# Performance work log

Measured on AMD Instinct MI355X. Metric: run time of the kernel, lower is better.

## Reference

```python
import jax, jax.numpy as jnp
import numpy as np

WS = 32      # window_size
P = 4        # patch size inside window
HEADS = 8
DIM_HEAD = 64
INNER = HEADS * DIM_HEAD  # 512
SCALE = DIM_HEAD ** -0.5


def setup_inputs() -> dict:
    key = jax.random.key(0)
    k1, k2, k3 = jax.random.split(key, 3)
    B, C, S = 8, 64, 256
    token_dim = P * P * C  # 1024
    x = jax.random.normal(k1, (B, C, S, S), dtype=jnp.float32)
    w_qkv = jax.random.normal(k2, (token_dim, 3 * INNER), dtype=jnp.float32) * (token_dim ** -0.5)
    w_out = jax.random.normal(k3, (INNER, token_dim), dtype=jnp.float32) * (INNER ** -0.5)
    b_out = jnp.zeros((token_dim,), dtype=jnp.float32)
    return {"x": x, "w_qkv": w_qkv, "w_out": w_out, "b_out": b_out}


def reference(x, w_qkv, w_out, b_out):
    B, C, H, W = x.shape
    H1, W1 = H // WS, W // WS
    # --- divide_regions: b c (h1 h) (w1 w) -> (b h1 w1) c h w ---
    xw = x.reshape(B, C, H1, WS, W1, WS).transpose(0, 2, 4, 1, 3, 5)
    xw = xw.reshape(B * H1 * W1, C, WS, WS)          # [n, C, ws, ws]
    n = xw.shape[0]
    nh = WS // P                                      # patches per side
    # patchify window: n c (nh p1) (nw p2) -> n (nh nw) (p1 p2 c)
    t = xw.reshape(n, C, nh, P, nh, P).transpose(0, 2, 4, 3, 5, 1)
    tokens = t.reshape(n, nh * nh, P * P * C)         # [n, T, D]
    # --- attention ---
    qkv = jnp.einsum('ntd,de->nte', tokens, w_qkv)    # [n, T, 3*inner]
    q, k, v = jnp.split(qkv, 3, axis=-1)
    def heads(a):
        return a.reshape(n, -1, HEADS, DIM_HEAD).transpose(0, 2, 1, 3)  # [n,h,T,dh]
    q, k, v = heads(q), heads(k), heads(v)
    attn = jax.nn.softmax(jnp.einsum('nhqd,nhkd->nhqk', q, k) * SCALE, axis=-1)
    o = jnp.einsum('nhqk,nhkd->nhqd', attn, v)        # [n,h,T,dh]
    o = o.transpose(0, 2, 1, 3).reshape(n, nh * nh, INNER)
    o = jnp.einsum('nte,ed->ntd', o, w_out) + b_out   # [n, T, D]
    # un-patchify: n (nh nw) (p1 p2 c) -> n c (nh p1) (nw p2)
    o = o.reshape(n, nh, nh, P, P, C).transpose(0, 5, 1, 3, 2, 4)
    o = o.reshape(n, C, WS, WS)
    # --- combine_regions: (b h1 w1) c h w -> b c (h1 h) (w1 w) ---
    o = o.reshape(B, H1, W1, C, WS, WS).transpose(0, 3, 1, 4, 2, 5)
    return o.reshape(B, C, H, W)
```

## Files before the change

### kernel.cpp

```cpp
#include <hip/hip_runtime.h>
#include <hip/hip_bf16.h>
#include <stdint.h>

typedef __attribute__((ext_vector_type(8))) short short8;
typedef __attribute__((ext_vector_type(4))) float floatx4;

constexpr int TD    = 1024;
constexpr int E3    = 1536;
constexpr int INNER = 512;
constexpr int NW    = 512;
constexpr int M_    = NW * 64;


constexpr size_t OFF_TOKA = 0;
constexpr size_t OFF_QKV  = (size_t)M_ * TD * 2;
constexpr size_t OFF_WQT  = OFF_QKV + (size_t)M_ * E3 * 2;
constexpr size_t OFF_WOT  = OFF_WQT + (size_t)E3 * TD * 2;
constexpr size_t OFF_BO   = OFF_WOT + (size_t)TD * INNER * 2;
constexpr size_t WS_NEED  = OFF_BO + TD * 4;

__device__ __forceinline__ void gl_lds16(const void* g, void* l) {
  __builtin_amdgcn_global_load_lds(
      (const __attribute__((address_space(1))) void*)g,
      (__attribute__((address_space(3))) void*)l, 16, 0, 0);
}

__global__ __launch_bounds__(256) void k_patchify(const float* __restrict__ x,
                                                  __hip_bfloat16* __restrict__ tokA) {
  __shared__ __hip_bfloat16 tok[8][1032];
  const int bid = blockIdx.x;
  const int n = bid >> 3, i = bid & 7;
  const int b = n >> 6, h1 = (n >> 3) & 7, w1 = n & 7;
  const int tid = threadIdx.x;
  for (int it = 0; it < 8; ++it) {
    int idx = it * 256 + tid;
    int w4 = idx & 7, p1 = (idx >> 3) & 3, c = idx >> 5;
    int h = h1 * 32 + i * 4 + p1;
    const float4 v = *(const float4*)&x[(((b * 64 + c) * 256 + h) * 256 + w1 * 32 + w4 * 4)];
    __hip_bfloat16* dst = &tok[w4][c * 16 + p1 * 4];
    dst[0] = __float2bfloat16(v.x);
    dst[1] = __float2bfloat16(v.y);
    dst[2] = __float2bfloat16(v.z);
    dst[3] = __float2bfloat16(v.w);
  }
  __syncthreads();
  for (int it = 0; it < 4; ++it) {
    int idx = it * 256 + tid;
    int ch = idx & 127, j = idx >> 7;
    uint4 v = *(const uint4*)&tok[j][ch * 8];
    *(uint4*)&tokA[(size_t)(n * 64 + i * 8 + j) * 1024 + ch * 8] = v;
  }
}

__global__ __launch_bounds__(256) void k_perm_wqkv(const float* __restrict__ wqkv,
                                                   __hip_bfloat16* __restrict__ wqT) {
  __shared__ __hip_bfloat16 wt[16][520];
  const int e0 = blockIdx.x * 16, by = blockIdx.y, tid = threadIdx.x;
  for (int it = 0; it < 32; ++it) {
    int idx = it * 256 + tid;
    int e = idx & 15, dl = idx >> 4;
    int d = by * 512 + dl;
    float v = wqkv[d * 1536 + e0 + e];
    int c = d & 63, off = (d >> 6) & 7;
    wt[e][c * 8 + off] = __float2bfloat16(v);
  }
  __syncthreads();
  for (int it = 0; it < 4; ++it) {
    int idx = it * 256 + tid;
    int ch = idx & 63, e = idx >> 6;
    uint4 v = *(const uint4*)&wt[e][ch * 8];
    *(uint4*)&wqT[(size_t)(e0 + e) * 1024 + ch * 16 + by * 8] = v;
  }
}

__global__ __launch_bounds__(256) void k_perm_wout(const float* __restrict__ wout,
                                                   __hip_bfloat16* __restrict__ woT) {
  __shared__ __hip_bfloat16 wt[4][520];
  const int e0 = blockIdx.x * 4, by = blockIdx.y, tid = threadIdx.x;
  for (int it = 0; it < 8; ++it) {
    int idx = it * 256 + tid;
    int dl = idx & 511, e = idx >> 9;
    int d = by * 512 + dl;
    float v = wout[(e0 + e) * 1024 + d];
    int c = d & 63, off = (d >> 6) & 7;
    wt[e][c * 8 + off] = __float2bfloat16(v);
  }
  __syncthreads();
  for (int it = 0; it < 8; ++it) {
    int idx = it * 256 + tid;
    int e = idx & 3, sl = idx >> 2;
    int c = sl >> 3, off = sl & 7;
    int dp = c * 16 + by * 8 + off;
    woT[(size_t)dp * 512 + e0 + e] = wt[e][sl];
  }
}

__global__ __launch_bounds__(256) void k_perm_bias(const float* __restrict__ bout,
                                                   float* __restrict__ boP) {
  int dp = blockIdx.x * 256 + threadIdx.x;
  int c = dp >> 4, p1 = (dp >> 2) & 3, p2 = dp & 3;
  boP[dp] = bout[p1 * 256 + p2 * 64 + c];
}

template<int K>
__device__ __forceinline__ void gemm256_acc(
    const __hip_bfloat16* __restrict__ A,
    const __hip_bfloat16* __restrict__ Bt,
    int m0, int n0, int tid,
    __hip_bfloat16 (*As)[256][64], __hip_bfloat16 (*Bs)[256][64],
    floatx4 (&acc)[8][4])
{
  const int lane = tid & 63, wid = tid >> 6;
  const int wm = wid >> 2, wn = wid & 3;
  const int l15 = lane & 15, quad = lane >> 4;

  const int rl8 = tid >> 3;
  const int ch0 = (tid & 7) ^ (rl8 & 7);
  const __hip_bfloat16* Abase = A  + (size_t)(m0 + rl8) * K + ch0 * 8;
  const __hip_bfloat16* Bbase = Bt + (size_t)(n0 + rl8) * K + ch0 * 8;

  auto stageB = [&](int tile, int half, int buf) {
#pragma unroll
    for (int j = 0; j < 2; ++j)
      gl_lds16(Bbase + (size_t)(half * 128 + j * 64) * K + tile * 64,
               (char*)&Bs[buf][0][0] + half * 16384 + (j * 512 + tid) * 16);
  };
  auto stageA = [&](int tile, int chunk, int buf) {
#pragma unroll
    for (int j = 0; j < 2; ++j)
      gl_lds16(Abase + (size_t)(j * 128 + chunk * 64) * K + tile * 64,
               (char*)&As[buf][0][0] + j * 16384 + chunk * 8192 + tid * 16);
  };

  short8 af[2][2][2];
  short8 bf[4][2];

#define VM6 asm volatile("s_waitcnt vmcnt(6)" ::: "memory")
#define VM0 asm volatile("s_waitcnt vmcnt(0)" ::: "memory")
#define LGKM4 do { asm volatile("s_waitcnt lgkmcnt(4)" ::: "memory"); \
                   __builtin_amdgcn_sched_barrier(0); } while (0)
#define LGKM0 do { asm volatile("s_waitcnt lgkmcnt(0)" ::: "memory"); \
                   __builtin_amdgcn_sched_barrier(0); } while (0)

#define PH(CS, QC, BUFC, LDB, QN, BUFN, PF, STAGE, VMW, LG)                       \
  do {                                                                            \
    if (LDB) {                              \
      _Pragma("unroll") for (int n = 0; n < 4; ++n) {                             \
        const int rb = wn * 64 + n * 16 + l15;                                    \
        _Pragma("unroll") for (int kh = 0; kh < 2; ++kh)                          \
          bf[n][kh] = *(const short8*)&Bs[BUFC][rb][((kh * 4 + quad) ^ (rb & 7)) * 8]; \
      }                                                                           \
    }                                                                             \
    if (PF) {                                                                     \
      _Pragma("unroll") for (int m2 = 0; m2 < 2; ++m2) {                          \
        const int r = wm * 128 + (2 * (QN) + m2) * 16 + l15;                      \
        _Pragma("unroll") for (int kh = 0; kh < 2; ++kh)                          \
          af[(CS) ^ 1][m2][kh] = *(const short8*)&As[BUFN][r][((kh * 4 + quad) ^ (r & 7)) * 8]; \
      }                                                                           \
    }                                                                             \
    STAGE;                                                                        \
    __builtin_amdgcn_sched_barrier(0);                                            \
    __builtin_amdgcn_s_barrier();                                                 \
    LG;                                                                           \
    __builtin_amdgcn_s_setprio(1);                                                \
    _Pragma("unroll") for (int kh = 0; kh < 2; ++kh)                              \
      _Pragma("unroll") for (int m2 = 0; m2 < 2; ++m2)                            \
        _Pragma("unroll") for (int n = 0; n < 4; ++n)                             \
          acc[2 * (QC) + m2][n] = __builtin_amdgcn_mfma_f32_16x16x32_bf16(        \
              af[CS][m2][kh], bf[n][kh], acc[2 * (QC) + m2][n], 0, 0, 0);         \
    __builtin_amdgcn_s_setprio(0);                                                \
    __builtin_amdgcn_sched_barrier(0);                                            \
    VMW;                                                                          \
    __builtin_amdgcn_s_barrier();                                                 \
    __builtin_amdgcn_sched_barrier(0);                                            \
  } while (0)

  stageB(0, 0, 0); stageB(0, 1, 0); stageA(0, 0, 0); stageA(0, 1, 0);
  stageB(1, 0, 1); stageB(1, 1, 1); stageA(1, 0, 1);
  VM6;
  __builtin_amdgcn_s_barrier();
  __builtin_amdgcn_sched_barrier(0);
#pragma unroll
  for (int m2 = 0; m2 < 2; ++m2) {
    const int r = wm * 128 + m2 * 16 + l15;
#pragma unroll
    for (int kh = 0; kh < 2; ++kh)
      af[0][m2][kh] = *(const short8*)&As[0][r][((kh * 4 + quad) ^ (r & 7)) * 8];
  }

  constexpr int NIT = K / 128;
#pragma unroll 1
  for (int i = 0; i < NIT - 1; ++i) {
    const int t1 = 2 * i + 1, t2 = 2 * i + 2, t3 = 2 * i + 3;
    PH(0, 0, 0, 1, 1, 0, 1, stageA(t1, 1, 1), VM6, LGKM4);
    PH(1, 1, 0, 0, 2, 0, 1, stageB(t2, 0, 0),    , LGKM4);
    PH(0, 2, 0, 0, 3, 0, 1, stageB(t2, 1, 0), VM6, LGKM4);
    PH(1, 3, 0, 0, 0, 1, 1, stageA(t2, 0, 0),    , LGKM4);
    PH(0, 0, 1, 1, 1, 1, 1, stageA(t2, 1, 0), VM6, LGKM4);
    PH(1, 1, 1, 0, 2, 1, 1, stageB(t3, 0, 1),    , LGKM4);
    PH(0, 2, 1, 0, 3, 1, 1, stageB(t3, 1, 1), VM6, LGKM4);
    PH(1, 3, 1, 0, 0, 0, 1, stageA(t3, 0, 1),    , LGKM4);
  }
  {
    const int tE = 2 * NIT - 1;
    PH(0, 0, 0, 1, 1, 0, 1, stageA(tE, 1, 1), VM6, LGKM4);
    PH(1, 1, 0, 0, 2, 0, 1, ,    , LGKM4);
    PH(0, 2, 0, 0, 3, 0, 1, , VM0, LGKM4);
    PH(1, 3, 0, 0, 0, 1, 1, ,    , LGKM4);
    PH(0, 0, 1, 1, 1, 1, 1, ,    , LGKM4);
    PH(1, 1, 1, 0, 2, 1, 1, ,    , LGKM4);
    PH(0, 2, 1, 0, 3, 1, 1, ,    , LGKM4);
    PH(1, 3, 1, 0, 0, 0, 0, ,    , LGKM0);
  }
#undef PH
#undef VM6
#undef VM0
#undef LGKM4
#undef LGKM0
}

__global__ __launch_bounds__(512, 2) void k_gemm_qkv(const __hip_bfloat16* __restrict__ A,
                                                     const __hip_bfloat16* __restrict__ Bt,
                                                     __hip_bfloat16* __restrict__ Cmat,
                                                     int lognb, int nbase) {
  __shared__ __hip_bfloat16 As[2][256][64];
  __shared__ __hip_bfloat16 Bs[2][256][64];
  const int tid = threadIdx.x;
  const int bid = blockIdx.x;
  const int cpx = gridDim.x >> 3;
  const int swz = (bid & 7) * cpx + (bid >> 3);
  const int nb1 = (1 << lognb) - 1;
  const int n0 = nbase + (swz & nb1) * 256, m0 = (swz >> lognb) * 256;
  floatx4 acc[8][4] = {};
  gemm256_acc<1024>(A, Bt, m0, n0, tid, As, Bs, acc);
  const int lane = tid & 63, wid = tid >> 6;
  const int wm = wid >> 2, wn = wid & 3;
  const int l15 = lane & 15, quad = lane >> 4;
#pragma unroll
  for (int mt = 0; mt < 8; ++mt)
#pragma unroll
    for (int nt = 0; nt < 4; ++nt) {
      const int col = n0 + wn * 64 + nt * 16 + l15;
#pragma unroll
      for (int r = 0; r < 4; ++r) {
        const int row = m0 + wm * 128 + mt * 16 + quad * 4 + r;
        Cmat[(size_t)row * 1536 + col] = __float2bfloat16(acc[mt][nt][r]);
      }
    }
}

__global__ __launch_bounds__(256) void k_attn(const __hip_bfloat16* __restrict__ qkv,
                                              __hip_bfloat16* __restrict__ oattn) {
  __shared__ __hip_bfloat16 Qs[64 * 64];
  __shared__ __hip_bfloat16 Ks[64 * 64];
  __shared__ __hip_bfloat16 Vt[64 * 72];
  __shared__ __hip_bfloat16 Ps[64 * 72];
  const int win = blockIdx.x, head = blockIdx.y;
  const int tid = threadIdx.x, lane = tid & 63, wid = tid >> 6;
  const int l15 = lane & 15, quad = lane >> 4;
  const int sx = l15 & 7;
  const size_t base = (size_t)win * 64 * 1536 + head * 64;
  for (int l = 0; l < 2; ++l) {
    int idx = l * 256 + tid;
    int t = idx >> 3, ch = idx & 7;
    const size_t rowb = base + (size_t)t * 1536 + ch * 8;
    uint4 q = *(const uint4*)&qkv[rowb];
    uint4 k = *(const uint4*)&qkv[rowb + 512];
    uint4 v = *(const uint4*)&qkv[rowb + 1024];
    const int pos = (ch ^ (t & 7)) * 8;
    *(uint4*)&Qs[t * 64 + pos] = q;
    *(uint4*)&Ks[t * 64 + pos] = k;
    *(uint4*)&Ps[t * 64 + pos] = v;
  }
  __syncthreads();
  {
    const int t = tid & 63, w = tid >> 6;
#pragma unroll
    for (int jn = 0; jn < 2; ++jn) {
      int j = w * 2 + jn;
      short8 v = *(const short8*)&Ps[t * 64 + ((j ^ (t & 7)) * 8)];
#pragma unroll
      for (int jj = 0; jj < 8; ++jj) Vt[(j * 8 + jj) * 72 + t] = ((__hip_bfloat16*)&v)[jj];
    }
  }
  __syncthreads();
  floatx4 sacc[4] = {};
#pragma unroll
  for (int kk = 0; kk < 64; kk += 32) {
    const int pos = (((kk >> 3) + quad) ^ sx) * 8;
    short8 aq = *(const short8*)&Qs[(wid * 16 + l15) * 64 + pos];
#pragma unroll
    for (int ct = 0; ct < 4; ++ct) {
      short8 bk = *(const short8*)&Ks[(ct * 16 + l15) * 64 + pos];
      sacc[ct] = __builtin_amdgcn_mfma_f32_16x16x32_bf16(aq, bk, sacc[ct], 0, 0, 0);
    }
  }
#pragma unroll
  for (int ct = 0; ct < 4; ++ct)
#pragma unroll
    for (int r = 0; r < 4; ++r) sacc[ct][r] = sacc[ct][r] * 0.125f;
#pragma unroll
  for (int r = 0; r < 4; ++r) {
    float m = fmaxf(fmaxf(sacc[0][r], sacc[1][r]), fmaxf(sacc[2][r], sacc[3][r]));
    m = fmaxf(m, __shfl_xor(m, 1));
    m = fmaxf(m, __shfl_xor(m, 2));
    m = fmaxf(m, __shfl_xor(m, 4));
    m = fmaxf(m, __shfl_xor(m, 8));
    float ev[4]; float s0 = 0.f;
#pragma unroll
    for (int ct = 0; ct < 4; ++ct) { ev[ct] = __expf(sacc[ct][r] - m); s0 += ev[ct]; }
    s0 += __shfl_xor(s0, 1);
    s0 += __shfl_xor(s0, 2);
    s0 += __shfl_xor(s0, 4);
    s0 += __shfl_xor(s0, 8);
    float inv = 1.0f / s0;
    int row = wid * 16 + quad * 4 + r;
#pragma unroll
    for (int ct = 0; ct < 4; ++ct)
      Ps[row * 72 + ct * 16 + l15] = __float2bfloat16(ev[ct] * inv);
  }
  __syncthreads();
  floatx4 oacc[4] = {};
#pragma unroll
  for (int kk = 0; kk < 64; kk += 32) {
    const int q8 = quad * 8;
    short8 ap = *(const short8*)&Ps[(wid * 16 + l15) * 72 + kk + q8];
#pragma unroll
    for (int nt = 0; nt < 4; ++nt) {
      short8 bv = *(const short8*)&Vt[(nt * 16 + l15) * 72 + kk + q8];
      oacc[nt] = __builtin_amdgcn_mfma_f32_16x16x32_bf16(ap, bv, oacc[nt], 0, 0, 0);
    }
  }
#pragma unroll
  for (int nt = 0; nt < 4; ++nt) {
    int dh = nt * 16 + l15;
#pragma unroll
    for (int r = 0; r < 4; ++r) {
      int t = wid * 16 + quad * 4 + r;
      oattn[((size_t)win * 64 + t) * 512 + head * 64 + dh] = __float2bfloat16(oacc[nt][r]);
    }
  }
}

__global__ __launch_bounds__(512, 2) void k_gemm_out(const __hip_bfloat16* __restrict__ A,
                                                     const __hip_bfloat16* __restrict__ Bt,
                                                     const float* __restrict__ bias,
                                                     float* __restrict__ out) {
  __shared__ __hip_bfloat16 As[2][256][64];
  __shared__ __hip_bfloat16 Bs[2][256][64];
  const int tid = threadIdx.x;
  const int bid = blockIdx.x;
  const int swz = (bid & 7) * 64 + (bid >> 3);
  const int n0 = (swz & 3) * 256, m0 = (swz >> 2) * 256;
  floatx4 acc[8][4] = {};
  gemm256_acc<512>(A, Bt, m0, n0, tid, As, Bs, acc);
  const int lane = tid & 63, wid = tid >> 6;
  const int wm = wid >> 2, wn = wid & 3;
  const int l15 = lane & 15, quad = lane >> 4;
#pragma unroll
  for (int nt = 0; nt < 4; ++nt) {
    const int dp = n0 + wn * 64 + nt * 16 + l15;
    const float bv = bias[dp];
    const int c = dp >> 4, p1 = (dp >> 2) & 3, p2 = dp & 3;
#pragma unroll
    for (int mt = 0; mt < 8; ++mt)
#pragma unroll
      for (int r = 0; r < 4; ++r) {
        const int m = m0 + wm * 128 + mt * 16 + quad * 4 + r;
        const int win = m >> 6, t = m & 63;
        const int i = t >> 3, j = t & 7;
        const int b = win >> 6, h1 = (win >> 3) & 7, w1 = win & 7;
        const int h = h1 * 32 + i * 4 + p1, w = w1 * 32 + j * 4 + p2;
        out[((b * 64 + c) * 256 + h) * 256 + w] = acc[mt][nt][r] + bv;
      }
  }
}

extern "C" void kernel_launch(void* const* d_in, const int* in_sizes, int n_in,
                              void* d_out, int out_size, void* d_ws, size_t ws_size,
                              hipStream_t stream) {
  const float* x    = (const float*)d_in[0];
  const float* wqkv = (const float*)d_in[1];
  const float* wout = (const float*)d_in[2];
  const float* bout = (const float*)d_in[3];
  float* out = (float*)d_out;
  char* ws = (char*)d_ws;
  if (ws_size < WS_NEED) return;

  __hip_bfloat16* tokA  = (__hip_bfloat16*)(ws + OFF_TOKA);
  __hip_bfloat16* oattn = (__hip_bfloat16*)(ws + OFF_TOKA);
  __hip_bfloat16* qkv   = (__hip_bfloat16*)(ws + OFF_QKV);
  __hip_bfloat16* wqT   = (__hip_bfloat16*)(ws + OFF_WQT);
  __hip_bfloat16* woT   = (__hip_bfloat16*)(ws + OFF_WOT);
  float* boP = (float*)(ws + OFF_BO);

  k_perm_wqkv<<<dim3(96, 2), 256, 0, stream>>>(wqkv, wqT);
  k_perm_wout<<<dim3(128, 2), 256, 0, stream>>>(wout, woT);
  k_perm_bias<<<4, 256, 0, stream>>>(bout, boP);
  k_patchify<<<4096, 256, 0, stream>>>(x, tokA);
  k_gemm_qkv<<<512, 512, 0, stream>>>(tokA, wqT, qkv, 2, 0);
  k_gemm_qkv<<<256, 512, 0, stream>>>(tokA, wqT, qkv, 1, 1024);
  k_attn<<<dim3(512, 8), 256, 0, stream>>>(qkv, oattn);
  k_gemm_out<<<512, 512, 0, stream>>>(oattn, woT, boP, out);
}
```

Measured before the change: 440.7 us.

## Restructure GEMM pipeline into per-tile groups and merge QKV launches

Rewrites the shared 256x256 GEMM main loop from an 8-phase, two-tile schedule into one group per K-tile. Each group has a single barrier and staging loads spread across four MFMA sub-phases, which removes many per-phase barriers. It also merges the two QKV GEMM launches into one 768-block grid with a fixed 6-column swizzle. The cost is fewer synchronization points, which raises the risk of LDS buffer hazards, and a full vmcnt(0) wait per tile that may expose load latency.

```diff
diff --git a/kernel.cpp b/kernel.cpp
--- a/kernel.cpp
+++ b/kernel.cpp
@@ -119,118 +119,109 @@
   const __hip_bfloat16* Abase = A  + (size_t)(m0 + rl8) * K + ch0 * 8;
   const __hip_bfloat16* Bbase = Bt + (size_t)(n0 + rl8) * K + ch0 * 8;
 
-  auto stageB = [&](int tile, int half, int buf) {
-#pragma unroll
-    for (int j = 0; j < 2; ++j)
-      gl_lds16(Bbase + (size_t)(half * 128 + j * 64) * K + tile * 64,
-               (char*)&Bs[buf][0][0] + half * 16384 + (j * 512 + tid) * 16);
+  auto stB = [&](int tile, int q, int buf) {
+    gl_lds16(Bbase + (size_t)(q * 64) * K + tile * 64,
+             (char*)&Bs[buf][0][0] + q * 8192 + tid * 16);
   };
-  auto stageA = [&](int tile, int chunk, int buf) {
-#pragma unroll
-    for (int j = 0; j < 2; ++j)
-      gl_lds16(Abase + (size_t)(j * 128 + chunk * 64) * K + tile * 64,
-               (char*)&As[buf][0][0] + j * 16384 + chunk * 8192 + tid * 16);
+  auto stA = [&](int tile, int chunk, int j, int buf) {
+    gl_lds16(Abase + (size_t)(j * 128 + chunk * 64) * K + tile * 64,
+             (char*)&As[buf][0][0] + j * 16384 + chunk * 8192 + tid * 16);
   };
 
   short8 af[2][2][2];
   short8 bf[4][2];
 
-#define VM6 asm volatile("s_waitcnt vmcnt(6)" ::: "memory")
-#define VM0 asm volatile("s_waitcnt vmcnt(0)" ::: "memory")
 #define LGKM4 do { asm volatile("s_waitcnt lgkmcnt(4)" ::: "memory"); \
                    __builtin_amdgcn_sched_barrier(0); } while (0)
-#define LGKM0 do { asm volatile("s_waitcnt lgkmcnt(0)" ::: "memory"); \
-                   __builtin_amdgcn_sched_barrier(0); } while (0)
-
-#define PH(CS, QC, BUFC, LDB, QN, BUFN, PF, STAGE, VMW, LG)                       \
+#define VM0   asm volatile("s_waitcnt vmcnt(0)" ::: "memory")
+#define VM6   asm volatile("s_waitcnt vmcnt(6)" ::: "memory")
+
+#define READ_AF(SET, Q, BUF)                                                      \
   do {                                                                            \
-    if (LDB) {                              \
-      _Pragma("unroll") for (int n = 0; n < 4; ++n) {                             \
-        const int rb = wn * 64 + n * 16 + l15;                                    \
-        _Pragma("unroll") for (int kh = 0; kh < 2; ++kh)                          \
-          bf[n][kh] = *(const short8*)&Bs[BUFC][rb][((kh * 4 + quad) ^ (rb & 7)) * 8]; \
-      }                                                                           \
+    _Pragma("unroll") for (int m2 = 0; m2 < 2; ++m2) {                            \
+      const int r = wm * 128 + (2 * (Q) + m2) * 16 + l15;                         \
+      _Pragma("unroll") for (int kh = 0; kh < 2; ++kh)                            \
+        af[SET][m2][kh] = *(const short8*)&As[BUF][r][((kh * 4 + quad) ^ (r & 7)) * 8]; \
     }                                                                             \
-    if (PF) {                                                                     \
-      _Pragma("unroll") for (int m2 = 0; m2 < 2; ++m2) {                          \
-        const int r = wm * 128 + (2 * (QN) + m2) * 16 + l15;                      \
-        _Pragma("unroll") for (int kh = 0; kh < 2; ++kh)                          \
-          af[(CS) ^ 1][m2][kh] = *(const short8*)&As[BUFN][r][((kh * 4 + quad) ^ (r & 7)) * 8]; \
-      }                                                                           \
-    }                                                                             \
-    STAGE;                                                                        \
-    __builtin_amdgcn_sched_barrier(0);                                            \
-    __builtin_amdgcn_s_barrier();                                                 \
-    LG;                                                                           \
+  } while (0)
+
+#define MFMA16(SET, Q)                                                            \
+  do {                                                                            \
     __builtin_amdgcn_s_setprio(1);                                                \
     _Pragma("unroll") for (int kh = 0; kh < 2; ++kh)                              \
       _Pragma("unroll") for (int m2 = 0; m2 < 2; ++m2)                            \
         _Pragma("unroll") for (int n = 0; n < 4; ++n)                             \
-          acc[2 * (QC) + m2][n] = __builtin_amdgcn_mfma_f32_16x16x32_bf16(        \
-              af[CS][m2][kh], bf[n][kh], acc[2 * (QC) + m2][n], 0, 0, 0);         \
+          acc[2 * (Q) + m2][n] = __builtin_amdgcn_mfma_f32_16x16x32_bf16(         \
+              af[SET][m2][kh], bf[n][kh], acc[2 * (Q) + m2][n], 0, 0, 0);         \
     __builtin_amdgcn_s_setprio(0);                                                \
     __builtin_amdgcn_sched_barrier(0);                                            \
-    VMW;                                                                          \
-    __builtin_amdgcn_s_barrier();                                                 \
-    __builtin_amdgcn_sched_barrier(0);                                            \
   } while (0)
 
-  stageB(0, 0, 0); stageB(0, 1, 0); stageA(0, 0, 0); stageA(0, 1, 0);
-  stageB(1, 0, 1); stageB(1, 1, 1); stageA(1, 0, 1);
+  constexpr int NT = K / 64;
+
+  stB(0, 0, 0); stB(0, 1, 0); stB(0, 2, 0); stB(0, 3, 0);
+  stA(0, 0, 0, 0); stA(0, 0, 1, 0);
+  stA(0, 1, 0, 0); stA(0, 1, 1, 0);
+  stB(1, 0, 1); stB(1, 1, 1); stB(1, 2, 1); stB(1, 3, 1);
+  stA(1, 0, 0, 1); stA(1, 0, 1, 1);
   VM6;
   __builtin_amdgcn_s_barrier();
   __builtin_amdgcn_sched_barrier(0);
-#pragma unroll
-  for (int m2 = 0; m2 < 2; ++m2) {
-    const int r = wm * 128 + m2 * 16 + l15;
-#pragma unroll
-    for (int kh = 0; kh < 2; ++kh)
-      af[0][m2][kh] = *(const short8*)&As[0][r][((kh * 4 + quad) ^ (r & 7)) * 8];
-  }
-
-  constexpr int NIT = K / 128;
-#pragma unroll 1
-  for (int i = 0; i < NIT - 1; ++i) {
-    const int t1 = 2 * i + 1, t2 = 2 * i + 2, t3 = 2 * i + 3;
-    PH(0, 0, 0, 1, 1, 0, 1, stageA(t1, 1, 1), VM6, LGKM4);
-    PH(1, 1, 0, 0, 2, 0, 1, stageB(t2, 0, 0),    , LGKM4);
-    PH(0, 2, 0, 0, 3, 0, 1, stageB(t2, 1, 0), VM6, LGKM4);
-    PH(1, 3, 0, 0, 0, 1, 1, stageA(t2, 0, 0),    , LGKM4);
-    PH(0, 0, 1, 1, 1, 1, 1, stageA(t2, 1, 0), VM6, LGKM4);
-    PH(1, 1, 1, 0, 2, 1, 1, stageB(t3, 0, 1),    , LGKM4);
-    PH(0, 2, 1, 0, 3, 1, 1, stageB(t3, 1, 1), VM6, LGKM4);
-    PH(1, 3, 1, 0, 0, 0, 1, stageA(t3, 0, 1),    , LGKM4);
-  }
-  {
-    const int tE = 2 * NIT - 1;
-    PH(0, 0, 0, 1, 1, 0, 1, stageA(tE, 1, 1), VM6, LGKM4);
-    PH(1, 1, 0, 0, 2, 0, 1, ,    , LGKM4);
-    PH(0, 2, 0, 0, 3, 0, 1, , VM0, LGKM4);
-    PH(1, 3, 0, 0, 0, 1, 1, ,    , LGKM4);
-    PH(0, 0, 1, 1, 1, 1, 1, ,    , LGKM4);
-    PH(1, 1, 1, 0, 2, 1, 1, ,    , LGKM4);
-    PH(0, 2, 1, 0, 3, 1, 1, ,    , LGKM4);
-    PH(1, 3, 1, 0, 0, 0, 0, ,    , LGKM0);
-  }
-#undef PH
+  READ_AF(0, 0, 0);
+
+#define GROUP(P, T)                                                               \
+  do {                                                                            \
+                             \
+    _Pragma("unroll") for (int n = 0; n < 4; ++n) {                               \
+      const int rb = wn * 64 + n * 16 + l15;                                      \
+      _Pragma("unroll") for (int kh = 0; kh < 2; ++kh)                            \
+        bf[n][kh] = *(const short8*)&Bs[P][rb][((kh * 4 + quad) ^ (rb & 7)) * 8]; \
+    }                                                                             \
+    READ_AF(1, 1, P);                                                             \
+    LGKM4;                                                                        \
+    MFMA16(0, 0);                                                                 \
+    VM0;                                                                          \
+    __builtin_amdgcn_s_barrier();                                                 \
+    __builtin_amdgcn_sched_barrier(0);                                            \
+                 \
+    READ_AF(0, 2, P);                                                             \
+    if ((T) + 1 < NT) { stA((T) + 1, 1, 0, (P) ^ 1); stA((T) + 1, 1, 1, (P) ^ 1); } \
+    if ((T) + 2 < NT) { stA((T) + 2, 0, 0, P); }                                  \
+    LGKM4;                                                                        \
+    MFMA16(1, 1);                                                                 \
+                      \
+    READ_AF(1, 3, P);                                                             \
+    if ((T) + 2 < NT) { stA((T) + 2, 0, 1, P); stB((T) + 2, 0, P); stB((T) + 2, 1, P); } \
+    LGKM4;                                                                        \
+    MFMA16(0, 2);                                                                 \
+                     \
+    if ((T) + 1 < NT) { READ_AF(0, 0, (P) ^ 1); }                                 \
+    if ((T) + 2 < NT) { stB((T) + 2, 2, P); stB((T) + 2, 3, P); }                 \
+    LGKM4;                                                                        \
+    MFMA16(1, 3);                                                                 \
+  } while (0)
+
+#pragma unroll 2
+  for (int t = 0; t < NT; ++t) {
+    if ((t & 1) == 0) GROUP(0, t); else GROUP(1, t);
+  }
+#undef GROUP
+#undef READ_AF
+#undef MFMA16
+#undef LGKM4
+#undef VM0
 #undef VM6
-#undef VM0
-#undef LGKM4
-#undef LGKM0
 }
 
 __global__ __launch_bounds__(512, 2) void k_gemm_qkv(const __hip_bfloat16* __restrict__ A,
                                                      const __hip_bfloat16* __restrict__ Bt,
-                                                     __hip_bfloat16* __restrict__ Cmat,
-                                                     int lognb, int nbase) {
+                                                     __hip_bfloat16* __restrict__ Cmat) {
   __shared__ __hip_bfloat16 As[2][256][64];
   __shared__ __hip_bfloat16 Bs[2][256][64];
   const int tid = threadIdx.x;
   const int bid = blockIdx.x;
-  const int cpx = gridDim.x >> 3;
-  const int swz = (bid & 7) * cpx + (bid >> 3);
-  const int nb1 = (1 << lognb) - 1;
-  const int n0 = nbase + (swz & nb1) * 256, m0 = (swz >> lognb) * 256;
+  const int swz = (bid & 7) * 96 + (bid >> 3);
+  const int n0 = (swz % 6) * 256, m0 = (swz / 6) * 256;
   floatx4 acc[8][4] = {};
   gemm256_acc<1024>(A, Bt, m0, n0, tid, As, Bs, acc);
   const int lane = tid & 63, wid = tid >> 6;
@@ -398,8 +389,7 @@
   k_perm_wout<<<dim3(128, 2), 256, 0, stream>>>(wout, woT);
   k_perm_bias<<<4, 256, 0, stream>>>(bout, boP);
   k_patchify<<<4096, 256, 0, stream>>>(x, tokA);
-  k_gemm_qkv<<<512, 512, 0, stream>>>(tokA, wqT, qkv, 2, 0);
-  k_gemm_qkv<<<256, 512, 0, stream>>>(tokA, wqT, qkv, 1, 1024);
+  k_gemm_qkv<<<768, 512, 0, stream>>>(tokA, wqT, qkv);
   k_attn<<<dim3(512, 8), 256, 0, stream>>>(qkv, oattn);
   k_gemm_out<<<512, 512, 0, stream>>>(oattn, woT, boP, out);
 }
```

Result: faster. 418.6 us (-5.0%).
